# Optimization experiments

Hardware: AMD Instinct MI355X
Metric: run time of the kernel (lower is better)

## Reference

```python
import jax, jax.numpy as jnp
import numpy as np

EPS = 1e-08
SIGMA = 0.1
B = 1.0


def setup_inputs() -> dict:
    key = jax.random.key(0)
    k1, k2 = jax.random.split(key)
    N, C, H, W = 4, 256, 64, 64
    featureT = jax.random.normal(k1, (N, C, H, W), dtype=jnp.float32)
    featureI = jax.random.normal(k2, (N, C, H, W), dtype=jnp.float32)
    return {"featureT": featureT, "featureI": featureI}


def reference(featureT, featureI):
    N, C, H, W = featureT.shape
    # center both by target mean over (batch, spatial)
    meanT = featureT.mean(axis=(0, 2, 3), keepdims=True)
    fI = featureI - meanT
    fT = featureT - meanT
    # channel-wise L2 normalize
    fI = fI / (jnp.linalg.norm(fI, axis=1, keepdims=True) + EPS)
    fT = fT / (jnp.linalg.norm(fT, axis=1, keepdims=True) + EPS)
    # 1x1-patch conv2d == contraction over channels: sim[n, p, h, w]
    # where p indexes the flattened H*W spatial positions of the target.
    fT_flat = fT.reshape(N, C, H * W)  # [N, C, P]
    sim = jnp.einsum('nchw,ncp->nphw', fI, fT_flat)  # [N, P, H, W]
    raw_dist = (1.0 - sim) / 2.0
    # relative distances: divide by min over patch axis
    div = jnp.min(raw_dist, axis=1, keepdims=True)
    relative_dist = raw_dist / (div + EPS)
    # contextual similarity: exp-weight + sum-normalize over patch axis
    Wt = jnp.exp((B - relative_dist) / (SIGMA + EPS))
    W_sum = Wt.sum(axis=1, keepdims=True)
    CX = Wt / (W_sum + EPS)
    # max over spatial dims of featureI, mean over patches, -log, mean over batch
    CX = CX.max(axis=(2, 3))           # [N, P]
    CX = CX.mean(axis=1)               # [N]
    CX_loss = -jnp.log(CX + EPS)
    return jnp.mean(CX_loss)
```

## Files before the change

kernel.cpp:

```cpp
#include <hip/hip_runtime.h>
#include <cmath>


#define NB 4
#define CC 256
#define HW 4096
#define NQ0 8
#define NCS 16

static constexpr float kEPS = 1e-8f;
static constexpr float kSIG = 0.1f + 1e-8f;

typedef __attribute__((ext_vector_type(8)))  short short8;
typedef __attribute__((ext_vector_type(16))) float f32x16;

enum {
  OFF_MEAN = 0,
  OFF_CMAX = 256,
  OFF_WSUM = OFF_CMAX + NQ0*NB*HW,
  OFF_MAXP = OFF_WSUM + NQ0*NB*HW,
  OFF_MAXV = OFF_MAXP + NCS*NB*HW,
  OFF_GB   = OFF_MAXV + NB*HW,
  OFF_GT   = OFF_GB + 2*NB*HW,
  OFF_GI   = OFF_GT + NB*HW*CC/2,
  WS_FLOATS_FULL = OFF_GI + NB*HW*CC/2
};

__device__ __forceinline__ ushort cvt_bf16(float x) {
  unsigned u = __float_as_uint(x);
  unsigned r = (u + 0x7fffu + ((u >> 16) & 1u)) >> 16;
  return (ushort)r;
}
__device__ __forceinline__ float bf2f(ushort u) {
  return __uint_as_float((unsigned)u << 16);
}

__device__ __forceinline__ float blockSum256(float v) {
  __shared__ float sh[4];
  const int lane = threadIdx.x & 63, wv = threadIdx.x >> 6;
  #pragma unroll
  for (int o = 32; o > 0; o >>= 1) v += __shfl_down(v, o, 64);
  __syncthreads();
  if (lane == 0) sh[wv] = v;
  __syncthreads();
  return sh[0] + sh[1] + sh[2] + sh[3];
}

__global__ __launch_bounds__(256) void k_mean9(const float* __restrict__ fT,
                                               float* __restrict__ ws) {
  const int c = blockIdx.x, t = threadIdx.x;
  float s = 0.f;
  for (int n = 0; n < NB; ++n) {
    const float* p = fT + (size_t)(n*CC + c)*HW;
    #pragma unroll
    for (int k = 0; k < 16; ++k) s += p[k*256 + t];
  }
  const float tot = blockSum256(s);
  if (t == 0) ws[OFF_MEAN + c] = tot * (1.0f/16384.0f);
}

__global__ __launch_bounds__(256) void k_prep9(const float* __restrict__ fT,
                                               const float* __restrict__ fI,
                                               float* __restrict__ ws) {
  __shared__ float stage[32][257];
  __shared__ float prt[8][32];
  __shared__ float sinv[32];
  const int t = threadIdx.x, l = t & 63;
  int bid = blockIdx.x;
  const int tensor = (bid >= 512); bid &= 511;
  const int n   = bid >> 7;
  const int r32 = bid & 127;
  const int p0  = r32 * 32;

  const float* __restrict__ src = tensor ? fI : fT;
  ushort* __restrict__ dst = (ushort*)(ws + (tensor ? OFF_GI : OFF_GT));
  const float* __restrict__ mean = ws + OFF_MEAN;

  const int pl = t & 31, cg = t >> 5;
  float acc = 0.f;
  #pragma unroll
  for (int i = 0; i < 32; ++i) {
    const int c = cg*32 + i;
    const float v = src[((size_t)(n*CC + c))*HW + p0 + pl] - mean[c];
    stage[pl][c] = v;
    acc += v*v;
  }
  prt[cg][pl] = acc;
  __syncthreads();
  if (t < 32) {
    float s = 0.f;
    #pragma unroll
    for (int g = 0; g < 8; ++g) s += prt[g][t];
    sinv[t] = 1.0f/(sqrtf(s) + kEPS);
  }
  __syncthreads();

  const int w = t >> 6, lhi = l >> 5, m = l & 31;
  const float iv = sinv[m];
  #pragma unroll
  for (int i = 0; i < 4; ++i) {
    const int kc = w*4 + i;
    const int cb = kc*16 + lhi*8;
    short8 o;
    #pragma unroll
    for (int j = 0; j < 8; ++j)
      ((ushort*)&o)[j] = cvt_bf16(stage[m][cb + j] * iv);
    *(short8*)(dst + (((size_t)(n*128 + r32)*16 + kc) << 9) + l*8) = o;
  }
}


__global__ __launch_bounds__(256, 2) void k_gA(
    const ushort* __restrict__ gA, const ushort* __restrict__ gB,
    float* __restrict__ ws)
{
  __shared__ ushort Ab[8192];
  __shared__ float red2[256];

  const int t = threadIdx.x;
  const int w = t >> 6, l = t & 63;
  const int ln31 = l & 31;

  const int b = blockIdx.x;
  const int h = b & 7, sid = b >> 3;
  const int n = sid >> 4;
  const int col0 = (sid & 15) * 256;

  const ushort* __restrict__ gAn = gA + (size_t)(n*128 + h*16)*8192;

  short8 pf[4];
  #pragma unroll
  for (int i = 0; i < 4; ++i)
    pf[i] = *(const short8*)(gAn + (size_t)(i*256 + t)*8);

  short8 breg0[16], breg1[16];
  {
    const int RB0 = (col0 >> 5) + w;
    const int RB1 = (col0 >> 5) + 4 + w;
    #pragma unroll
    for (int kc = 0; kc < 16; ++kc) {
      breg0[kc] = *(const short8*)(gB + (((size_t)(n*128 + RB0)*16 + kc) << 9) + l*8);
      breg1[kc] = *(const short8*)(gB + (((size_t)(n*128 + RB1)*16 + kc) << 9) + l*8);
    }
  }

  float run0 = -3.0e38f, run1 = -3.0e38f;

  for (int iter = 0; iter < 16; ++iter) {
    __syncthreads();
    #pragma unroll
    for (int i = 0; i < 4; ++i)
      *(short8*)&Ab[(i*256 + t)*8] = pf[i];
    __syncthreads();
    if (iter + 1 < 16) {
      const ushort* __restrict__ src = gAn + (size_t)(iter + 1)*8192;
      #pragma unroll
      for (int i = 0; i < 4; ++i)
        pf[i] = *(const short8*)(src + (size_t)(i*256 + t)*8);
    }

    f32x16 acc0, acc1;
    #pragma unroll
    for (int e = 0; e < 16; ++e) { acc0[e] = 0.f; acc1[e] = 0.f; }
    #pragma unroll
    for (int kc = 0; kc < 16; ++kc) {
      const short8 a0 = *(const short8*)&Ab[kc*512 + l*8];
      acc0 = __builtin_amdgcn_mfma_f32_32x32x16_bf16(a0, breg0[kc], acc0, 0, 0, 0);
      acc1 = __builtin_amdgcn_mfma_f32_32x32x16_bf16(a0, breg1[kc], acc1, 0, 0, 0);
    }
    #pragma unroll
    for (int r = 0; r < 16; ++r) {
      run0 = fmaxf(run0, acc0[r]);
      run1 = fmaxf(run1, acc1[r]);
    }
  }

  run0 = fmaxf(run0, __shfl_xor(run0, 32, 64));
  run1 = fmaxf(run1, __shfl_xor(run1, 32, 64));
  if (l < 32) {
    red2[w*32 + ln31]       = run0;
    red2[128 + w*32 + ln31] = run1;
  }
  __syncthreads();
  ws[OFF_CMAX + h*(NB*HW) + n*HW + col0 + t] = red2[t];
}

__global__ __launch_bounds__(256, 2) void k_gB(
    const ushort* __restrict__ gA, const ushort* __restrict__ gB,
    float* __restrict__ ws)
{
  __shared__ ushort Ab[8192];
  __shared__ float red2[256];

  const int t = threadIdx.x;
  const int w = t >> 6, l = t & 63;
  const int ln31 = l & 31;

  const int b = blockIdx.x;
  const int h = b & 7, sid = b >> 3;
  const int n = sid >> 4;
  const int col0 = (sid & 15) * 256;

  float aq0, bq0, aq1, bq1;
  {
    const int q0 = col0 + w*32 + ln31;
    const int q1 = q0 + 128;
    float cm0 = -3.0e38f, cm1 = -3.0e38f;
    #pragma unroll
    for (int hh = 0; hh < NQ0; ++hh) {
      cm0 = fmaxf(cm0, ws[OFF_CMAX + hh*(NB*HW) + n*HW + q0]);
      cm1 = fmaxf(cm1, ws[OFF_CMAX + hh*(NB*HW) + n*HW + q1]);
    }
    const float i0 = 1.0f/(2.0f*(0.5f*(1.0f - cm0) + kEPS));
    const float i1 = 1.0f/(2.0f*(0.5f*(1.0f - cm1) + kEPS));
    bq0 = i0 / kSIG; aq0 = (1.0f - i0) / kSIG;
    bq1 = i1 / kSIG; aq1 = (1.0f - i1) / kSIG;
  }

  const ushort* __restrict__ gAn = gA + (size_t)(n*128 + h*16)*8192;

  short8 pf[4];
  #pragma unroll
  for (int i = 0; i < 4; ++i)
    pf[i] = *(const short8*)(gAn + (size_t)(i*256 + t)*8);

  short8 breg0[16], breg1[16];
  {
    const int RB0 = (col0 >> 5) + w;
    const int RB1 = (col0 >> 5) + 4 + w;
    #pragma unroll
    for (int kc = 0; kc < 16; ++kc) {
      breg0[kc] = *(const short8*)(gB + (((size_t)(n*128 + RB0)*16 + kc) << 9) + l*8);
      breg1[kc] = *(const short8*)(gB + (((size_t)(n*128 + RB1)*16 + kc) << 9) + l*8);
    }
  }

  float ws0 = 0.f, ws1 = 0.f;

  for (int iter = 0; iter < 16; ++iter) {
    __syncthreads();
    #pragma unroll
    for (int i = 0; i < 4; ++i)
      *(short8*)&Ab[(i*256 + t)*8] = pf[i];
    __syncthreads();
    if (iter + 1 < 16) {
      const ushort* __restrict__ src = gAn + (size_t)(iter + 1)*8192;
      #pragma unroll
      for (int i = 0; i < 4; ++i)
        pf[i] = *(const short8*)(src + (size_t)(i*256 + t)*8);
    }

    f32x16 acc0, acc1;
    #pragma unroll
    for (int e = 0; e < 16; ++e) { acc0[e] = 0.f; acc1[e] = 0.f; }
    #pragma unroll
    for (int kc = 0; kc < 16; ++kc) {
      const short8 a0 = *(const short8*)&Ab[kc*512 + l*8];
      acc0 = __builtin_amdgcn_mfma_f32_32x32x16_bf16(a0, breg0[kc], acc0, 0, 0, 0);
      acc1 = __builtin_amdgcn_mfma_f32_32x32x16_bf16(a0, breg1[kc], acc1, 0, 0, 0);
    }
    #pragma unroll
    for (int r = 0; r < 16; ++r) {
      ws0 += __expf(fmaf(bq0, acc0[r], aq0));
      ws1 += __expf(fmaf(bq1, acc1[r], aq1));
    }
  }

  ws0 += __shfl_xor(ws0, 32, 64);
  ws1 += __shfl_xor(ws1, 32, 64);
  if (l < 32) {
    red2[w*32 + ln31]       = ws0;
    red2[128 + w*32 + ln31] = ws1;
  }
  __syncthreads();
  ws[OFF_WSUM + h*(NB*HW) + n*HW + col0 + t] = red2[t];
}

__global__ __launch_bounds__(256) void k_gb9(float* __restrict__ ws) {
  const int idx = blockIdx.x*256 + threadIdx.x;
  float cm = -3.0e38f;
  #pragma unroll
  for (int hh = 0; hh < NQ0; ++hh)
    cm = fmaxf(cm, ws[OFF_CMAX + hh*(NB*HW) + idx]);
  const float inv2d = 1.0f/(2.0f*(0.5f*(1.0f - cm) + kEPS));
  const float beta  = inv2d / kSIG;
  const float alpha = (1.0f - inv2d) / kSIG;
  float sw = 0.f;
  #pragma unroll
  for (int hh = 0; hh < NQ0; ++hh)
    sw += ws[OFF_WSUM + hh*(NB*HW) + idx];
  ws[OFF_GB + idx]         = alpha - logf(sw + kEPS);
  ws[OFF_GB + NB*HW + idx] = beta;
}

__global__ __launch_bounds__(256, 2) void k_gC(
    const ushort* __restrict__ gA, const ushort* __restrict__ gB,
    float* __restrict__ ws)
{
  __shared__ ushort Ab[8192];
  __shared__ float Ef[32*264];

  const int t = threadIdx.x;
  const int w = t >> 6, l = t & 63;
  const int ln31 = l & 31, lhi = l >> 5;

  const int b = blockIdx.x;
  const int h = b & 7, sid = b >> 3;
  const int n = sid >> 4;
  const int cs = sid & 15;
  const int col0 = cs * 256;

  float gq0, bq0, gq1, bq1;
  {
    const int q0 = col0 + w*32 + ln31;
    const int q1 = q0 + 128;
    gq0 = ws[OFF_GB + n*HW + q0];
    bq0 = ws[OFF_GB + NB*HW + n*HW + q0];
    gq1 = ws[OFF_GB + n*HW + q1];
    bq1 = ws[OFF_GB + NB*HW + n*HW + q1];
  }

  const ushort* __restrict__ gAn = gA + (size_t)(n*128 + h*16)*8192;

  short8 pf[4];
  #pragma unroll
  for (int i = 0; i < 4; ++i)
    pf[i] = *(const short8*)(gAn + (size_t)(i*256 + t)*8);

  short8 breg0[16], breg1[16];
  {
    const int RB0 = (col0 >> 5) + w;
    const int RB1 = (col0 >> 5) + 4 + w;
    #pragma unroll
    for (int kc = 0; kc < 16; ++kc) {
      breg0[kc] = *(const short8*)(gB + (((size_t)(n*128 + RB0)*16 + kc) << 9) + l*8);
      breg1[kc] = *(const short8*)(gB + (((size_t)(n*128 + RB1)*16 + kc) << 9) + l*8);
    }
  }

  const int ecol = w*32 + ln31;
  const int lr = t >> 3, qc = (t & 7) * 32;
  float* __restrict__ MAXP = ws + OFF_MAXP + (size_t)cs*(NB*HW) + n*HW;

  for (int iter = 0; iter < 16; ++iter) {
    __syncthreads();
    #pragma unroll
    for (int i = 0; i < 4; ++i)
      *(short8*)&Ab[(i*256 + t)*8] = pf[i];
    __syncthreads();
    if (iter + 1 < 16) {
      const ushort* __restrict__ src = gAn + (size_t)(iter + 1)*8192;
      #pragma unroll
      for (int i = 0; i < 4; ++i)
        pf[i] = *(const short8*)(src + (size_t)(i*256 + t)*8);
    }

    f32x16 acc0, acc1;
    #pragma unroll
    for (int e = 0; e < 16; ++e) { acc0[e] = 0.f; acc1[e] = 0.f; }
    #pragma unroll
    for (int kc = 0; kc < 16; ++kc) {
      const short8 a0 = *(const short8*)&Ab[kc*512 + l*8];
      acc0 = __builtin_amdgcn_mfma_f32_32x32x16_bf16(a0, breg0[kc], acc0, 0, 0, 0);
      acc1 = __builtin_amdgcn_mfma_f32_32x32x16_bf16(a0, breg1[kc], acc1, 0, 0, 0);
    }

    #pragma unroll
    for (int r = 0; r < 16; ++r) {
      const int lrow = 4*lhi + (r & 3) + 8*(r >> 2);
      Ef[lrow*264 + ecol]       = fmaf(bq0, acc0[r], gq0);
      Ef[lrow*264 + 128 + ecol] = fmaf(bq1, acc1[r], gq1);
    }
    __syncthreads();

    float m = -3.0e38f;
    #pragma unroll
    for (int k4 = 0; k4 < 8; ++k4) {
      const float4 v = *(const float4*)&Ef[lr*264 + qc + 4*k4];
      m = fmaxf(m, fmaxf(fmaxf(v.x, v.y), fmaxf(v.z, v.w)));
    }
    m = fmaxf(m, __shfl_xor(m, 1, 64));
    m = fmaxf(m, __shfl_xor(m, 2, 64));
    m = fmaxf(m, __shfl_xor(m, 4, 64));
    if ((t & 7) == 0) MAXP[h*512 + iter*32 + lr] = m;
  }
}

__global__ __launch_bounds__(256) void k_red(float* __restrict__ ws) {
  const int idx = blockIdx.x*256 + threadIdx.x;
  float m = ws[OFF_MAXP + idx];
  #pragma unroll
  for (int cs = 1; cs < NCS; ++cs)
    m = fmaxf(m, ws[OFF_MAXP + cs*(NB*HW) + idx]);
  ws[OFF_MAXV + idx] = m;
}

__global__ __launch_bounds__(256) void k_final9(const float* __restrict__ ws,
                                                float* __restrict__ out) {
  const int t = threadIdx.x;
  float loss = 0.f;
  for (int n = 0; n < NB; ++n) {
    float s = 0.f;
    for (int k = 0; k < 16; ++k)
      s += __expf(ws[OFF_MAXV + n*HW + k*256 + t]);
    const float tot = blockSum256(s);
    loss += -logf(tot*(1.0f/4096.0f) + kEPS);
  }
  if (t == 0) out[0] = loss*0.25f;
}

extern "C" void kernel_launch(void* const* d_in, const int* in_sizes, int n_in,
                              void* d_out, int out_size, void* d_ws, size_t ws_size,
                              hipStream_t stream) {
  const float* fT = (const float*)d_in[0];
  const float* fI = (const float*)d_in[1];
  float* out = (float*)d_out;
  float* ws  = (float*)d_ws;

  const size_t need_full = (size_t)WS_FLOATS_FULL * sizeof(float);
  if (ws_size < need_full) return;

  const ushort* GT = (const ushort*)(ws + OFF_GT);
  const ushort* GI = (const ushort*)(ws + OFF_GI);
  k_mean9 <<<256,  256, 0, stream>>>(fT, ws);
  k_prep9 <<<1024, 256, 0, stream>>>(fT, fI, ws);
  k_gA    <<<512,  256, 0, stream>>>(GT, GI, ws);
  k_gB    <<<512,  256, 0, stream>>>(GT, GI, ws);
  k_gb9   <<<64,   256, 0, stream>>>(ws);
  k_gC    <<<512,  256, 0, stream>>>(GT, GI, ws);
  k_red   <<<64,   256, 0, stream>>>(ws);
  k_final9<<<1,    256, 0, stream>>>(ws, out);
}
```

Measured before the change: 197.2 us.

## Double-buffer A tiles via direct global-to-LDS loads, remap blocks per XCD, fuse gb9

The three GEMM-style kernels now use two LDS buffers filled by direct global-to-LDS loads issued two iterations ahead, replacing the register prefetch plus LDS store. Synchronisation moves to explicit vmcnt/lgkmcnt waits and raw s_barrier. Block indices are remapped so each XCD handles a contiguous group of column slices, aiming for better L2 reuse of the B operand. The small k_gb9 kernel is folded into k_gC's prologue, removing one launch at the cost of each block recomputing its gamma/beta. The hand-written waits risk ordering bugs if the compiler's instruction counts differ from the expected vmcnt(4).

```diff
diff --git a/kernel.cpp b/kernel.cpp
--- a/kernel.cpp
+++ b/kernel.cpp
@@ -20,8 +20,7 @@
   OFF_WSUM = OFF_CMAX + NQ0*NB*HW,
   OFF_MAXP = OFF_WSUM + NQ0*NB*HW,
   OFF_MAXV = OFF_MAXP + NCS*NB*HW,
-  OFF_GB   = OFF_MAXV + NB*HW,
-  OFF_GT   = OFF_GB + 2*NB*HW,
+  OFF_GT   = OFF_MAXV + NB*HW,
   OFF_GI   = OFF_GT + NB*HW*CC/2,
   WS_FLOATS_FULL = OFF_GI + NB*HW*CC/2
 };
@@ -31,9 +30,16 @@
   unsigned r = (u + 0x7fffu + ((u >> 16) & 1u)) >> 16;
   return (ushort)r;
 }
-__device__ __forceinline__ float bf2f(ushort u) {
-  return __uint_as_float((unsigned)u << 16);
-}
+
+__device__ __forceinline__ void glds16(const ushort* g, ushort* l) {
+  __builtin_amdgcn_global_load_lds(
+      (const __attribute__((address_space(1))) unsigned*)g,
+      (__attribute__((address_space(3))) unsigned*)l, 16, 0, 0);
+}
+__device__ __forceinline__ void s_bar()  { asm volatile("s_barrier" ::: "memory"); }
+__device__ __forceinline__ void w_vm4()  { asm volatile("s_waitcnt vmcnt(4)" ::: "memory"); }
+__device__ __forceinline__ void w_vm0()  { asm volatile("s_waitcnt vmcnt(0)" ::: "memory"); }
+__device__ __forceinline__ void w_lgkm() { asm volatile("s_waitcnt lgkmcnt(0)" ::: "memory"); }
 
 __device__ __forceinline__ float blockSum256(float v) {
   __shared__ float sh[4];
@@ -114,24 +120,28 @@
     const ushort* __restrict__ gA, const ushort* __restrict__ gB,
     float* __restrict__ ws)
 {
-  __shared__ ushort Ab[8192];
+  __shared__ ushort Ab[2][8192];
   __shared__ float red2[256];
 
   const int t = threadIdx.x;
   const int w = t >> 6, l = t & 63;
   const int ln31 = l & 31;
 
-  const int b = blockIdx.x;
-  const int h = b & 7, sid = b >> 3;
+  const int L = blockIdx.x;
+  const int xcd = L & 7, j = L >> 3;
+  const int sid = xcd*8 + (j & 7);
+  const int h   = j >> 3;
   const int n = sid >> 4;
   const int col0 = (sid & 15) * 256;
 
   const ushort* __restrict__ gAn = gA + (size_t)(n*128 + h*16)*8192;
 
-  short8 pf[4];
-  #pragma unroll
-  for (int i = 0; i < 4; ++i)
-    pf[i] = *(const short8*)(gAn + (size_t)(i*256 + t)*8);
+  #pragma unroll
+  for (int i = 0; i < 4; ++i)
+    glds16(gAn + (size_t)(i*256 + t)*8, &Ab[0][(i*256 + t)*8]);
+  #pragma unroll
+  for (int i = 0; i < 4; ++i)
+    glds16(gAn + 8192 + (size_t)(i*256 + t)*8, &Ab[1][(i*256 + t)*8]);
 
   short8 breg0[16], breg1[16];
   {
@@ -147,27 +157,29 @@
   float run0 = -3.0e38f, run1 = -3.0e38f;
 
   for (int iter = 0; iter < 16; ++iter) {
-    __syncthreads();
-    #pragma unroll
-    for (int i = 0; i < 4; ++i)
-      *(short8*)&Ab[(i*256 + t)*8] = pf[i];
-    __syncthreads();
-    if (iter + 1 < 16) {
-      const ushort* __restrict__ src = gAn + (size_t)(iter + 1)*8192;
+    if (iter < 15) w_vm4(); else w_vm0();
+    s_bar();
+
+    const ushort* __restrict__ Abuf = &Ab[iter & 1][0];
+    f32x16 acc0, acc1;
+    #pragma unroll
+    for (int e = 0; e < 16; ++e) { acc0[e] = 0.f; acc1[e] = 0.f; }
+    #pragma unroll
+    for (int kc = 0; kc < 16; ++kc) {
+      const short8 a0 = *(const short8*)&Abuf[kc*512 + l*8];
+      acc0 = __builtin_amdgcn_mfma_f32_32x32x16_bf16(a0, breg0[kc], acc0, 0, 0, 0);
+      acc1 = __builtin_amdgcn_mfma_f32_32x32x16_bf16(a0, breg1[kc], acc1, 0, 0, 0);
+    }
+    w_lgkm();
+    s_bar();
+    if (iter + 2 < 16) {
+      const ushort* __restrict__ src = gAn + (size_t)(iter + 2)*8192;
+      ushort* __restrict__ dstl = &Ab[iter & 1][0];
       #pragma unroll
       for (int i = 0; i < 4; ++i)
-        pf[i] = *(const short8*)(src + (size_t)(i*256 + t)*8);
-    }
-
-    f32x16 acc0, acc1;
-    #pragma unroll
-    for (int e = 0; e < 16; ++e) { acc0[e] = 0.f; acc1[e] = 0.f; }
-    #pragma unroll
-    for (int kc = 0; kc < 16; ++kc) {
-      const short8 a0 = *(const short8*)&Ab[kc*512 + l*8];
-      acc0 = __builtin_amdgcn_mfma_f32_32x32x16_bf16(a0, breg0[kc], acc0, 0, 0, 0);
-      acc1 = __builtin_amdgcn_mfma_f32_32x32x16_bf16(a0, breg1[kc], acc1, 0, 0, 0);
-    }
+        glds16(src + (size_t)(i*256 + t)*8, dstl + (i*256 + t)*8);
+    }
+
     #pragma unroll
     for (int r = 0; r < 16; ++r) {
       run0 = fmaxf(run0, acc0[r]);
@@ -189,17 +201,28 @@
     const ushort* __restrict__ gA, const ushort* __restrict__ gB,
     float* __restrict__ ws)
 {
-  __shared__ ushort Ab[8192];
+  __shared__ ushort Ab[2][8192];
   __shared__ float red2[256];
 
   const int t = threadIdx.x;
   const int w = t >> 6, l = t & 63;
   const int ln31 = l & 31;
 
-  const int b = blockIdx.x;
-  const int h = b & 7, sid = b >> 3;
+  const int L = blockIdx.x;
+  const int xcd = L & 7, j = L >> 3;
+  const int sid = xcd*8 + (j & 7);
+  const int h   = j >> 3;
   const int n = sid >> 4;
   const int col0 = (sid & 15) * 256;
+
+  const ushort* __restrict__ gAn = gA + (size_t)(n*128 + h*16)*8192;
+
+  #pragma unroll
+  for (int i = 0; i < 4; ++i)
+    glds16(gAn + (size_t)(i*256 + t)*8, &Ab[0][(i*256 + t)*8]);
+  #pragma unroll
+  for (int i = 0; i < 4; ++i)
+    glds16(gAn + 8192 + (size_t)(i*256 + t)*8, &Ab[1][(i*256 + t)*8]);
 
   float aq0, bq0, aq1, bq1;
   {
@@ -217,13 +240,6 @@
     bq1 = i1 / kSIG; aq1 = (1.0f - i1) / kSIG;
   }
 
-  const ushort* __restrict__ gAn = gA + (size_t)(n*128 + h*16)*8192;
-
-  short8 pf[4];
-  #pragma unroll
-  for (int i = 0; i < 4; ++i)
-    pf[i] = *(const short8*)(gAn + (size_t)(i*256 + t)*8);
-
   short8 breg0[16], breg1[16];
   {
     const int RB0 = (col0 >> 5) + w;
@@ -238,27 +254,29 @@
   float ws0 = 0.f, ws1 = 0.f;
 
   for (int iter = 0; iter < 16; ++iter) {
-    __syncthreads();
-    #pragma unroll
-    for (int i = 0; i < 4; ++i)
-      *(short8*)&Ab[(i*256 + t)*8] = pf[i];
-    __syncthreads();
-    if (iter + 1 < 16) {
-      const ushort* __restrict__ src = gAn + (size_t)(iter + 1)*8192;
+    if (iter < 15) w_vm4(); else w_vm0();
+    s_bar();
+
+    const ushort* __restrict__ Abuf = &Ab[iter & 1][0];
+    f32x16 acc0, acc1;
+    #pragma unroll
+    for (int e = 0; e < 16; ++e) { acc0[e] = 0.f; acc1[e] = 0.f; }
+    #pragma unroll
+    for (int kc = 0; kc < 16; ++kc) {
+      const short8 a0 = *(const short8*)&Abuf[kc*512 + l*8];
+      acc0 = __builtin_amdgcn_mfma_f32_32x32x16_bf16(a0, breg0[kc], acc0, 0, 0, 0);
+      acc1 = __builtin_amdgcn_mfma_f32_32x32x16_bf16(a0, breg1[kc], acc1, 0, 0, 0);
+    }
+    w_lgkm();
+    s_bar();
+    if (iter + 2 < 16) {
+      const ushort* __restrict__ src = gAn + (size_t)(iter + 2)*8192;
+      ushort* __restrict__ dstl = &Ab[iter & 1][0];
       #pragma unroll
       for (int i = 0; i < 4; ++i)
-        pf[i] = *(const short8*)(src + (size_t)(i*256 + t)*8);
-    }
-
-    f32x16 acc0, acc1;
-    #pragma unroll
-    for (int e = 0; e < 16; ++e) { acc0[e] = 0.f; acc1[e] = 0.f; }
-    #pragma unroll
-    for (int kc = 0; kc < 16; ++kc) {
-      const short8 a0 = *(const short8*)&Ab[kc*512 + l*8];
-      acc0 = __builtin_amdgcn_mfma_f32_32x32x16_bf16(a0, breg0[kc], acc0, 0, 0, 0);
-      acc1 = __builtin_amdgcn_mfma_f32_32x32x16_bf16(a0, breg1[kc], acc1, 0, 0, 0);
-    }
+        glds16(src + (size_t)(i*256 + t)*8, dstl + (i*256 + t)*8);
+    }
+
     #pragma unroll
     for (int r = 0; r < 16; ++r) {
       ws0 += __expf(fmaf(bq0, acc0[r], aq0));
@@ -276,56 +294,55 @@
   ws[OFF_WSUM + h*(NB*HW) + n*HW + col0 + t] = red2[t];
 }
 
-__global__ __launch_bounds__(256) void k_gb9(float* __restrict__ ws) {
-  const int idx = blockIdx.x*256 + threadIdx.x;
-  float cm = -3.0e38f;
-  #pragma unroll
-  for (int hh = 0; hh < NQ0; ++hh)
-    cm = fmaxf(cm, ws[OFF_CMAX + hh*(NB*HW) + idx]);
-  const float inv2d = 1.0f/(2.0f*(0.5f*(1.0f - cm) + kEPS));
-  const float beta  = inv2d / kSIG;
-  const float alpha = (1.0f - inv2d) / kSIG;
-  float sw = 0.f;
-  #pragma unroll
-  for (int hh = 0; hh < NQ0; ++hh)
-    sw += ws[OFF_WSUM + hh*(NB*HW) + idx];
-  ws[OFF_GB + idx]         = alpha - logf(sw + kEPS);
-  ws[OFF_GB + NB*HW + idx] = beta;
-}
-
 __global__ __launch_bounds__(256, 2) void k_gC(
     const ushort* __restrict__ gA, const ushort* __restrict__ gB,
     float* __restrict__ ws)
 {
-  __shared__ ushort Ab[8192];
+  __shared__ ushort Ab[2][8192];
   __shared__ float Ef[32*264];
+  __shared__ float gam[256], bet[256];
 
   const int t = threadIdx.x;
   const int w = t >> 6, l = t & 63;
   const int ln31 = l & 31, lhi = l >> 5;
 
-  const int b = blockIdx.x;
-  const int h = b & 7, sid = b >> 3;
+  const int L = blockIdx.x;
+  const int xcd = L & 7, j = L >> 3;
+  const int sid = xcd*8 + (j & 7);
+  const int h   = j >> 3;
   const int n = sid >> 4;
   const int cs = sid & 15;
   const int col0 = cs * 256;
 
-  float gq0, bq0, gq1, bq1;
   {
-    const int q0 = col0 + w*32 + ln31;
-    const int q1 = q0 + 128;
-    gq0 = ws[OFF_GB + n*HW + q0];
-    bq0 = ws[OFF_GB + NB*HW + n*HW + q0];
-    gq1 = ws[OFF_GB + n*HW + q1];
-    bq1 = ws[OFF_GB + NB*HW + n*HW + q1];
-  }
+    const int idx = n*HW + col0 + t;
+    float cm = -3.0e38f;
+    #pragma unroll
+    for (int hh = 0; hh < NQ0; ++hh)
+      cm = fmaxf(cm, ws[OFF_CMAX + hh*(NB*HW) + idx]);
+    const float inv2d = 1.0f/(2.0f*(0.5f*(1.0f - cm) + kEPS));
+    const float beta  = inv2d / kSIG;
+    const float alpha = (1.0f - inv2d) / kSIG;
+    float sw = 0.f;
+    #pragma unroll
+    for (int hh = 0; hh < NQ0; ++hh)
+      sw += ws[OFF_WSUM + hh*(NB*HW) + idx];
+    gam[t] = alpha - logf(sw + kEPS);
+    bet[t] = beta;
+  }
+  __syncthreads();
+
+  const float gq0 = gam[w*32 + ln31],       bq0 = bet[w*32 + ln31];
+  const float gq1 = gam[128 + w*32 + ln31], bq1 = bet[128 + w*32 + ln31];
 
   const ushort* __restrict__ gAn = gA + (size_t)(n*128 + h*16)*8192;
 
-  short8 pf[4];
-  #pragma unroll
-  for (int i = 0; i < 4; ++i)
-    pf[i] = *(const short8*)(gAn + (size_t)(i*256 + t)*8);
+  #pragma unroll
+  for (int i = 0; i < 4; ++i)
+    glds16(gAn + (size_t)(i*256 + t)*8, &Ab[0][(i*256 + t)*8]);
+  #pragma unroll
+  for (int i = 0; i < 4; ++i)
+    glds16(gAn + 8192 + (size_t)(i*256 + t)*8, &Ab[1][(i*256 + t)*8]);
 
   short8 breg0[16], breg1[16];
   {
@@ -343,24 +360,17 @@
   float* __restrict__ MAXP = ws + OFF_MAXP + (size_t)cs*(NB*HW) + n*HW;
 
   for (int iter = 0; iter < 16; ++iter) {
-    __syncthreads();
-    #pragma unroll
-    for (int i = 0; i < 4; ++i)
-      *(short8*)&Ab[(i*256 + t)*8] = pf[i];
-    __syncthreads();
-    if (iter + 1 < 16) {
-      const ushort* __restrict__ src = gAn + (size_t)(iter + 1)*8192;
-      #pragma unroll
-      for (int i = 0; i < 4; ++i)
-        pf[i] = *(const short8*)(src + (size_t)(i*256 + t)*8);
-    }
-
+    if (iter < 15) w_vm4(); else w_vm0();
+    w_lgkm();
+    s_bar();
+
+    const ushort* __restrict__ Abuf = &Ab[iter & 1][0];
     f32x16 acc0, acc1;
     #pragma unroll
     for (int e = 0; e < 16; ++e) { acc0[e] = 0.f; acc1[e] = 0.f; }
     #pragma unroll
     for (int kc = 0; kc < 16; ++kc) {
-      const short8 a0 = *(const short8*)&Ab[kc*512 + l*8];
+      const short8 a0 = *(const short8*)&Abuf[kc*512 + l*8];
       acc0 = __builtin_amdgcn_mfma_f32_32x32x16_bf16(a0, breg0[kc], acc0, 0, 0, 0);
       acc1 = __builtin_amdgcn_mfma_f32_32x32x16_bf16(a0, breg1[kc], acc1, 0, 0, 0);
     }
@@ -371,7 +381,15 @@
       Ef[lrow*264 + ecol]       = fmaf(bq0, acc0[r], gq0);
       Ef[lrow*264 + 128 + ecol] = fmaf(bq1, acc1[r], gq1);
     }
-    __syncthreads();
+    w_lgkm();
+    s_bar();
+    if (iter + 2 < 16) {
+      const ushort* __restrict__ src = gAn + (size_t)(iter + 2)*8192;
+      ushort* __restrict__ dstl = &Ab[iter & 1][0];
+      #pragma unroll
+      for (int i = 0; i < 4; ++i)
+        glds16(src + (size_t)(i*256 + t)*8, dstl + (i*256 + t)*8);
+    }
 
     float m = -3.0e38f;
     #pragma unroll
@@ -426,7 +444,6 @@
   k_prep9 <<<1024, 256, 0, stream>>>(fT, fI, ws);
   k_gA    <<<512,  256, 0, stream>>>(GT, GI, ws);
   k_gB    <<<512,  256, 0, stream>>>(GT, GI, ws);
-  k_gb9   <<<64,   256, 0, stream>>>(ws);
   k_gC    <<<512,  256, 0, stream>>>(GT, GI, ws);
   k_red   <<<64,   256, 0, stream>>>(ws);
   k_final9<<<1,    256, 0, stream>>>(ws, out);
```

Result: faster. 182.4 us (-7.5%).

## Stream A fragments straight to registers, drop LDS staging, fold gb9 into gC

Applied to the files above, without the earlier changes.

The three GEMM kernels now load the A operand directly from global memory into per-lane registers, prefetching the next tile inside the MFMA loop, so the LDS staging and both barriers per iteration are gone. Blocks are remapped so that blocks sharing an (n,h) A slice land on the same XCD, which should improve L2 reuse. The k_gb9 kernel is removed and its alpha/beta/log-sum computation is folded into k_gC's prologue, which saves a launch. The LDS max reduction in k_gC becomes a cross-lane shuffle reduction that writes per-wave partial maxima, which grows the MAXP buffer fourfold and makes k_red read 64 slices instead of 16. Register pressure rises and the occupancy hint is removed.

```diff
diff --git a/kernel.cpp b/kernel.cpp
--- a/kernel.cpp
+++ b/kernel.cpp
@@ -6,7 +6,7 @@
 #define CC 256
 #define HW 4096
 #define NQ0 8
-#define NCS 16
+#define NST 64
 
 static constexpr float kEPS = 1e-8f;
 static constexpr float kSIG = 0.1f + 1e-8f;
@@ -19,9 +19,8 @@
   OFF_CMAX = 256,
   OFF_WSUM = OFF_CMAX + NQ0*NB*HW,
   OFF_MAXP = OFF_WSUM + NQ0*NB*HW,
-  OFF_MAXV = OFF_MAXP + NCS*NB*HW,
-  OFF_GB   = OFF_MAXV + NB*HW,
-  OFF_GT   = OFF_GB + 2*NB*HW,
+  OFF_MAXV = OFF_MAXP + NST*NB*HW,
+  OFF_GT   = OFF_MAXV + NB*HW,
   OFF_GI   = OFF_GT + NB*HW*CC/2,
   WS_FLOATS_FULL = OFF_GI + NB*HW*CC/2
 };
@@ -30,9 +29,6 @@
   unsigned u = __float_as_uint(x);
   unsigned r = (u + 0x7fffu + ((u >> 16) & 1u)) >> 16;
   return (ushort)r;
-}
-__device__ __forceinline__ float bf2f(ushort u) {
-  return __uint_as_float((unsigned)u << 16);
 }
 
 __device__ __forceinline__ float blockSum256(float v) {
@@ -110,33 +106,26 @@
 }
 
 
-__global__ __launch_bounds__(256, 2) void k_gA(
+__global__ __launch_bounds__(256) void k_gA(
     const ushort* __restrict__ gA, const ushort* __restrict__ gB,
     float* __restrict__ ws)
 {
-  __shared__ ushort Ab[8192];
-  __shared__ float red2[256];
-
   const int t = threadIdx.x;
   const int w = t >> 6, l = t & 63;
   const int ln31 = l & 31;
 
-  const int b = blockIdx.x;
-  const int h = b & 7, sid = b >> 3;
-  const int n = sid >> 4;
-  const int col0 = (sid & 15) * 256;
-
-  const ushort* __restrict__ gAn = gA + (size_t)(n*128 + h*16)*8192;
-
-  short8 pf[4];
-  #pragma unroll
-  for (int i = 0; i < 4; ++i)
-    pf[i] = *(const short8*)(gAn + (size_t)(i*256 + t)*8);
+  const int L = blockIdx.x;
+  const int xcd = L & 7, g = L >> 3;
+  const int nh = xcd*4 + (g & 3);
+  const int cs = g >> 2;
+  const int n = nh >> 3, h = nh & 7;
+  const int col0 = cs * 256;
+
+  const ushort* __restrict__ gAf = gA + ((size_t)(n*128 + h*16) << 13);
 
   short8 breg0[16], breg1[16];
   {
-    const int RB0 = (col0 >> 5) + w;
-    const int RB1 = (col0 >> 5) + 4 + w;
+    const int RB0 = cs*8 + w, RB1 = cs*8 + 4 + w;
     #pragma unroll
     for (int kc = 0; kc < 16; ++kc) {
       breg0[kc] = *(const short8*)(gB + (((size_t)(n*128 + RB0)*16 + kc) << 9) + l*8);
@@ -144,29 +133,23 @@
     }
   }
 
+  short8 af[16];
+  #pragma unroll
+  for (int kc = 0; kc < 16; ++kc)
+    af[kc] = *(const short8*)(gAf + (kc << 9) + l*8);
+
   float run0 = -3.0e38f, run1 = -3.0e38f;
 
   for (int iter = 0; iter < 16; ++iter) {
-    __syncthreads();
-    #pragma unroll
-    for (int i = 0; i < 4; ++i)
-      *(short8*)&Ab[(i*256 + t)*8] = pf[i];
-    __syncthreads();
-    if (iter + 1 < 16) {
-      const ushort* __restrict__ src = gAn + (size_t)(iter + 1)*8192;
-      #pragma unroll
-      for (int i = 0; i < 4; ++i)
-        pf[i] = *(const short8*)(src + (size_t)(i*256 + t)*8);
-    }
-
     f32x16 acc0, acc1;
     #pragma unroll
     for (int e = 0; e < 16; ++e) { acc0[e] = 0.f; acc1[e] = 0.f; }
     #pragma unroll
     for (int kc = 0; kc < 16; ++kc) {
-      const short8 a0 = *(const short8*)&Ab[kc*512 + l*8];
-      acc0 = __builtin_amdgcn_mfma_f32_32x32x16_bf16(a0, breg0[kc], acc0, 0, 0, 0);
-      acc1 = __builtin_amdgcn_mfma_f32_32x32x16_bf16(a0, breg1[kc], acc1, 0, 0, 0);
+      acc0 = __builtin_amdgcn_mfma_f32_32x32x16_bf16(af[kc], breg0[kc], acc0, 0, 0, 0);
+      acc1 = __builtin_amdgcn_mfma_f32_32x32x16_bf16(af[kc], breg1[kc], acc1, 0, 0, 0);
+      if (iter < 15)
+        af[kc] = *(const short8*)(gAf + (((iter + 1)*16 + kc) << 9) + l*8);
     }
     #pragma unroll
     for (int r = 0; r < 16; ++r) {
@@ -178,28 +161,26 @@
   run0 = fmaxf(run0, __shfl_xor(run0, 32, 64));
   run1 = fmaxf(run1, __shfl_xor(run1, 32, 64));
   if (l < 32) {
-    red2[w*32 + ln31]       = run0;
-    red2[128 + w*32 + ln31] = run1;
-  }
-  __syncthreads();
-  ws[OFF_CMAX + h*(NB*HW) + n*HW + col0 + t] = red2[t];
-}
-
-__global__ __launch_bounds__(256, 2) void k_gB(
+    float* __restrict__ C = ws + OFF_CMAX + h*(NB*HW) + n*HW + col0 + w*32 + l;
+    C[0]   = run0;
+    C[128] = run1;
+  }
+}
+
+__global__ __launch_bounds__(256) void k_gB(
     const ushort* __restrict__ gA, const ushort* __restrict__ gB,
     float* __restrict__ ws)
 {
-  __shared__ ushort Ab[8192];
-  __shared__ float red2[256];
-
   const int t = threadIdx.x;
   const int w = t >> 6, l = t & 63;
   const int ln31 = l & 31;
 
-  const int b = blockIdx.x;
-  const int h = b & 7, sid = b >> 3;
-  const int n = sid >> 4;
-  const int col0 = (sid & 15) * 256;
+  const int L = blockIdx.x;
+  const int xcd = L & 7, g = L >> 3;
+  const int nh = xcd*4 + (g & 3);
+  const int cs = g >> 2;
+  const int n = nh >> 3, h = nh & 7;
+  const int col0 = cs * 256;
 
   float aq0, bq0, aq1, bq1;
   {
@@ -217,17 +198,11 @@
     bq1 = i1 / kSIG; aq1 = (1.0f - i1) / kSIG;
   }
 
-  const ushort* __restrict__ gAn = gA + (size_t)(n*128 + h*16)*8192;
-
-  short8 pf[4];
-  #pragma unroll
-  for (int i = 0; i < 4; ++i)
-    pf[i] = *(const short8*)(gAn + (size_t)(i*256 + t)*8);
+  const ushort* __restrict__ gAf = gA + ((size_t)(n*128 + h*16) << 13);
 
   short8 breg0[16], breg1[16];
   {
-    const int RB0 = (col0 >> 5) + w;
-    const int RB1 = (col0 >> 5) + 4 + w;
+    const int RB0 = cs*8 + w, RB1 = cs*8 + 4 + w;
     #pragma unroll
     for (int kc = 0; kc < 16; ++kc) {
       breg0[kc] = *(const short8*)(gB + (((size_t)(n*128 + RB0)*16 + kc) << 9) + l*8);
@@ -235,29 +210,23 @@
     }
   }
 
+  short8 af[16];
+  #pragma unroll
+  for (int kc = 0; kc < 16; ++kc)
+    af[kc] = *(const short8*)(gAf + (kc << 9) + l*8);
+
   float ws0 = 0.f, ws1 = 0.f;
 
   for (int iter = 0; iter < 16; ++iter) {
-    __syncthreads();
-    #pragma unroll
-    for (int i = 0; i < 4; ++i)
-      *(short8*)&Ab[(i*256 + t)*8] = pf[i];
-    __syncthreads();
-    if (iter + 1 < 16) {
-      const ushort* __restrict__ src = gAn + (size_t)(iter + 1)*8192;
-      #pragma unroll
-      for (int i = 0; i < 4; ++i)
-        pf[i] = *(const short8*)(src + (size_t)(i*256 + t)*8);
-    }
-
     f32x16 acc0, acc1;
     #pragma unroll
     for (int e = 0; e < 16; ++e) { acc0[e] = 0.f; acc1[e] = 0.f; }
     #pragma unroll
     for (int kc = 0; kc < 16; ++kc) {
-      const short8 a0 = *(const short8*)&Ab[kc*512 + l*8];
-      acc0 = __builtin_amdgcn_mfma_f32_32x32x16_bf16(a0, breg0[kc], acc0, 0, 0, 0);
-      acc1 = __builtin_amdgcn_mfma_f32_32x32x16_bf16(a0, breg1[kc], acc1, 0, 0, 0);
+      acc0 = __builtin_amdgcn_mfma_f32_32x32x16_bf16(af[kc], breg0[kc], acc0, 0, 0, 0);
+      acc1 = __builtin_amdgcn_mfma_f32_32x32x16_bf16(af[kc], breg1[kc], acc1, 0, 0, 0);
+      if (iter < 15)
+        af[kc] = *(const short8*)(gAf + (((iter + 1)*16 + kc) << 9) + l*8);
     }
     #pragma unroll
     for (int r = 0; r < 16; ++r) {
@@ -269,68 +238,56 @@
   ws0 += __shfl_xor(ws0, 32, 64);
   ws1 += __shfl_xor(ws1, 32, 64);
   if (l < 32) {
-    red2[w*32 + ln31]       = ws0;
-    red2[128 + w*32 + ln31] = ws1;
-  }
-  __syncthreads();
-  ws[OFF_WSUM + h*(NB*HW) + n*HW + col0 + t] = red2[t];
-}
-
-__global__ __launch_bounds__(256) void k_gb9(float* __restrict__ ws) {
-  const int idx = blockIdx.x*256 + threadIdx.x;
-  float cm = -3.0e38f;
-  #pragma unroll
-  for (int hh = 0; hh < NQ0; ++hh)
-    cm = fmaxf(cm, ws[OFF_CMAX + hh*(NB*HW) + idx]);
-  const float inv2d = 1.0f/(2.0f*(0.5f*(1.0f - cm) + kEPS));
-  const float beta  = inv2d / kSIG;
-  const float alpha = (1.0f - inv2d) / kSIG;
-  float sw = 0.f;
-  #pragma unroll
-  for (int hh = 0; hh < NQ0; ++hh)
-    sw += ws[OFF_WSUM + hh*(NB*HW) + idx];
-  ws[OFF_GB + idx]         = alpha - logf(sw + kEPS);
-  ws[OFF_GB + NB*HW + idx] = beta;
-}
-
-__global__ __launch_bounds__(256, 2) void k_gC(
+    float* __restrict__ W = ws + OFF_WSUM + h*(NB*HW) + n*HW + col0 + w*32 + l;
+    W[0]   = ws0;
+    W[128] = ws1;
+  }
+}
+
+__global__ __launch_bounds__(256) void k_gC(
     const ushort* __restrict__ gA, const ushort* __restrict__ gB,
     float* __restrict__ ws)
 {
-  __shared__ ushort Ab[8192];
-  __shared__ float Ef[32*264];
-
   const int t = threadIdx.x;
   const int w = t >> 6, l = t & 63;
   const int ln31 = l & 31, lhi = l >> 5;
 
-  const int b = blockIdx.x;
-  const int h = b & 7, sid = b >> 3;
-  const int n = sid >> 4;
-  const int cs = sid & 15;
+  const int L = blockIdx.x;
+  const int xcd = L & 7, g = L >> 3;
+  const int nh = xcd*4 + (g & 3);
+  const int cs = g >> 2;
+  const int n = nh >> 3, h = nh & 7;
   const int col0 = cs * 256;
 
   float gq0, bq0, gq1, bq1;
   {
     const int q0 = col0 + w*32 + ln31;
     const int q1 = q0 + 128;
-    gq0 = ws[OFF_GB + n*HW + q0];
-    bq0 = ws[OFF_GB + NB*HW + n*HW + q0];
-    gq1 = ws[OFF_GB + n*HW + q1];
-    bq1 = ws[OFF_GB + NB*HW + n*HW + q1];
-  }
-
-  const ushort* __restrict__ gAn = gA + (size_t)(n*128 + h*16)*8192;
-
-  short8 pf[4];
-  #pragma unroll
-  for (int i = 0; i < 4; ++i)
-    pf[i] = *(const short8*)(gAn + (size_t)(i*256 + t)*8);
+    float cm0 = -3.0e38f, cm1 = -3.0e38f;
+    #pragma unroll
+    for (int hh = 0; hh < NQ0; ++hh) {
+      cm0 = fmaxf(cm0, ws[OFF_CMAX + hh*(NB*HW) + n*HW + q0]);
+      cm1 = fmaxf(cm1, ws[OFF_CMAX + hh*(NB*HW) + n*HW + q1]);
+    }
+    float sw0 = 0.f, sw1 = 0.f;
+    #pragma unroll
+    for (int hh = 0; hh < NQ0; ++hh) {
+      sw0 += ws[OFF_WSUM + hh*(NB*HW) + n*HW + q0];
+      sw1 += ws[OFF_WSUM + hh*(NB*HW) + n*HW + q1];
+    }
+    const float i0 = 1.0f/(2.0f*(0.5f*(1.0f - cm0) + kEPS));
+    const float i1 = 1.0f/(2.0f*(0.5f*(1.0f - cm1) + kEPS));
+    bq0 = i0 / kSIG;
+    bq1 = i1 / kSIG;
+    gq0 = (1.0f - i0) / kSIG - logf(sw0 + kEPS);
+    gq1 = (1.0f - i1) / kSIG - logf(sw1 + kEPS);
+  }
+
+  const ushort* __restrict__ gAf = gA + ((size_t)(n*128 + h*16) << 13);
 
   short8 breg0[16], breg1[16];
   {
-    const int RB0 = (col0 >> 5) + w;
-    const int RB1 = (col0 >> 5) + 4 + w;
+    const int RB0 = cs*8 + w, RB1 = cs*8 + 4 + w;
     #pragma unroll
     for (int kc = 0; kc < 16; ++kc) {
       breg0[kc] = *(const short8*)(gB + (((size_t)(n*128 + RB0)*16 + kc) << 9) + l*8);
@@ -338,60 +295,47 @@
     }
   }
 
-  const int ecol = w*32 + ln31;
-  const int lr = t >> 3, qc = (t & 7) * 32;
-  float* __restrict__ MAXP = ws + OFF_MAXP + (size_t)cs*(NB*HW) + n*HW;
+  short8 af[16];
+  #pragma unroll
+  for (int kc = 0; kc < 16; ++kc)
+    af[kc] = *(const short8*)(gAf + (kc << 9) + l*8);
+
+  float* __restrict__ MAXP =
+      ws + OFF_MAXP + (size_t)(cs*4 + w)*(NB*HW) + n*HW;
 
   for (int iter = 0; iter < 16; ++iter) {
-    __syncthreads();
-    #pragma unroll
-    for (int i = 0; i < 4; ++i)
-      *(short8*)&Ab[(i*256 + t)*8] = pf[i];
-    __syncthreads();
-    if (iter + 1 < 16) {
-      const ushort* __restrict__ src = gAn + (size_t)(iter + 1)*8192;
-      #pragma unroll
-      for (int i = 0; i < 4; ++i)
-        pf[i] = *(const short8*)(src + (size_t)(i*256 + t)*8);
-    }
-
     f32x16 acc0, acc1;
     #pragma unroll
     for (int e = 0; e < 16; ++e) { acc0[e] = 0.f; acc1[e] = 0.f; }
     #pragma unroll
     for (int kc = 0; kc < 16; ++kc) {
-      const short8 a0 = *(const short8*)&Ab[kc*512 + l*8];
-      acc0 = __builtin_amdgcn_mfma_f32_32x32x16_bf16(a0, breg0[kc], acc0, 0, 0, 0);
-      acc1 = __builtin_amdgcn_mfma_f32_32x32x16_bf16(a0, breg1[kc], acc1, 0, 0, 0);
-    }
-
+      acc0 = __builtin_amdgcn_mfma_f32_32x32x16_bf16(af[kc], breg0[kc], acc0, 0, 0, 0);
+      acc1 = __builtin_amdgcn_mfma_f32_32x32x16_bf16(af[kc], breg1[kc], acc1, 0, 0, 0);
+      if (iter < 15)
+        af[kc] = *(const short8*)(gAf + (((iter + 1)*16 + kc) << 9) + l*8);
+    }
+
+    const int pb = h*512 + iter*32 + 4*lhi;
     #pragma unroll
     for (int r = 0; r < 16; ++r) {
-      const int lrow = 4*lhi + (r & 3) + 8*(r >> 2);
-      Ef[lrow*264 + ecol]       = fmaf(bq0, acc0[r], gq0);
-      Ef[lrow*264 + 128 + ecol] = fmaf(bq1, acc1[r], gq1);
-    }
-    __syncthreads();
-
-    float m = -3.0e38f;
-    #pragma unroll
-    for (int k4 = 0; k4 < 8; ++k4) {
-      const float4 v = *(const float4*)&Ef[lr*264 + qc + 4*k4];
-      m = fmaxf(m, fmaxf(fmaxf(v.x, v.y), fmaxf(v.z, v.w)));
-    }
-    m = fmaxf(m, __shfl_xor(m, 1, 64));
-    m = fmaxf(m, __shfl_xor(m, 2, 64));
-    m = fmaxf(m, __shfl_xor(m, 4, 64));
-    if ((t & 7) == 0) MAXP[h*512 + iter*32 + lr] = m;
+      float v = fmaxf(fmaf(bq0, acc0[r], gq0), fmaf(bq1, acc1[r], gq1));
+      v = fmaxf(v, __shfl_xor(v, 1, 64));
+      v = fmaxf(v, __shfl_xor(v, 2, 64));
+      v = fmaxf(v, __shfl_xor(v, 4, 64));
+      v = fmaxf(v, __shfl_xor(v, 8, 64));
+      v = fmaxf(v, __shfl_xor(v, 16, 64));
+      if (ln31 == 0)
+        MAXP[pb + (r & 3) + 8*(r >> 2)] = v;
+    }
   }
 }
 
 __global__ __launch_bounds__(256) void k_red(float* __restrict__ ws) {
   const int idx = blockIdx.x*256 + threadIdx.x;
   float m = ws[OFF_MAXP + idx];
-  #pragma unroll
-  for (int cs = 1; cs < NCS; ++cs)
-    m = fmaxf(m, ws[OFF_MAXP + cs*(NB*HW) + idx]);
+  #pragma unroll 8
+  for (int s = 1; s < NST; ++s)
+    m = fmaxf(m, ws[OFF_MAXP + s*(NB*HW) + idx]);
   ws[OFF_MAXV + idx] = m;
 }
 
@@ -426,7 +370,6 @@
   k_prep9 <<<1024, 256, 0, stream>>>(fT, fI, ws);
   k_gA    <<<512,  256, 0, stream>>>(GT, GI, ws);
   k_gB    <<<512,  256, 0, stream>>>(GT, GI, ws);
-  k_gb9   <<<64,   256, 0, stream>>>(ws);
   k_gC    <<<512,  256, 0, stream>>>(GT, GI, ws);
   k_red   <<<64,   256, 0, stream>>>(ws);
   k_final9<<<1,    256, 0, stream>>>(ws, out);
```

Result: slower. 269.4 us (+36.6%).
